# Performance work log

Measured on AMD Instinct MI355X. Metric: run time of the kernel, lower is better.

## Reference

```python
import jax, jax.numpy as jnp
import numpy as np

B, S, HID = 2, 2048, 2048
NH, NKV, HD = 32, 8, 64
ROPE_THETA = 10000.0
SCALE = HD ** -0.5
GROUP = NH // NKV


def setup_inputs() -> dict:
    key = jax.random.key(0)
    k1, k2, k3 = jax.random.split(key, 3)
    positions = jnp.tile(jnp.arange(S, dtype=jnp.int32), (B, 1))  # [B,S]
    hidden_states = jax.random.normal(k1, (B, S, HID), dtype=jnp.float32)
    Wqkv = jax.random.normal(k2, (HID, (NH + 2 * NKV) * HD), dtype=jnp.float32) * (HID ** -0.5)
    Wo = jax.random.normal(k3, (NH * HD, HID), dtype=jnp.float32) * ((NH * HD) ** -0.5)
    return {"positions": positions, "hidden_states": hidden_states, "Wqkv": Wqkv, "Wo": Wo}


def _apply_rope(x, cos, sin):
    # x: [B,S,H,HD]; cos/sin: [B,S,1,HD/2]  (neox style: rotate halves)
    x1, x2 = x[..., : HD // 2], x[..., HD // 2 :]
    return jnp.concatenate([x1 * cos - x2 * sin, x2 * cos + x1 * sin], axis=-1)


def reference(positions, hidden_states, Wqkv, Wo):
    # QKV projection (bias=False)
    qkv = hidden_states @ Wqkv  # [B,S,(NH+2*NKV)*HD]
    q, k, v = jnp.split(qkv, [NH * HD, (NH + NKV) * HD], axis=-1)
    q = q.reshape(B, S, NH, HD)
    k = k.reshape(B, S, NKV, HD)
    v = v.reshape(B, S, NKV, HD)

    # neox-style RoPE
    inv_freq = 1.0 / (ROPE_THETA ** (jnp.arange(0, HD, 2, dtype=jnp.float32) / HD))  # [HD/2]
    freqs = positions.astype(jnp.float32)[..., None] * inv_freq  # [B,S,HD/2]
    cos = jnp.cos(freqs)[:, :, None, :]
    sin = jnp.sin(freqs)[:, :, None, :]
    q = _apply_rope(q, cos, sin)
    k = _apply_rope(k, cos, sin)

    # GQA: expand KV heads to match query heads
    k = jnp.repeat(k, GROUP, axis=2)  # [B,S,NH,HD]
    v = jnp.repeat(v, GROUP, axis=2)

    # causal attention
    scores = jnp.einsum("bqhd,bkhd->bhqk", q, k) * SCALE  # [B,NH,S,S]
    causal = jnp.tril(jnp.ones((S, S), dtype=bool))
    scores = jnp.where(causal, scores, jnp.finfo(scores.dtype).min)
    probs = jax.nn.softmax(scores, axis=-1)
    attn = jnp.einsum("bhqk,bkhd->bqhd", probs, v).reshape(B, S, NH * HD)

    return attn @ Wo  # [B,S,HID]
```

## Files before the change

kernel.cpp:

```cpp
#include <hip/hip_runtime.h>
#include <hip/hip_bf16.h>
#include <math.h>

#define SEQ 2048
#define HIDDEN 2048
#define NHEAD 32
#define NKVH 8
#define HD 64
#define QKVW 3072

typedef __bf16 bf16_t;
typedef __bf16 bf16x8 __attribute__((ext_vector_type(8)));
typedef __bf16 bf16x4 __attribute__((ext_vector_type(4)));
typedef float f32x4 __attribute__((ext_vector_type(4)));

__device__ __forceinline__ void gld_lds16(const bf16_t* g, bf16_t* l) {
  __builtin_amdgcn_global_load_lds((const __attribute__((address_space(1))) void*)g,
                                   (__attribute__((address_space(3))) void*)l, 16, 0, 0);
}

__global__ __launch_bounds__(256) void k_fill(float* __restrict__ out, int n, float v) {
  int i = blockIdx.x * 256 + threadIdx.x;
  if (i < n) out[i] = v;
}

__global__ __launch_bounds__(256) void k_cvt(const float* __restrict__ in,
                                             bf16_t* __restrict__ out, int n4) {
  int i = blockIdx.x * 256 + threadIdx.x;
  if (i >= n4) return;
  float4 v = ((const float4*)in)[i];
  bf16x4 o;
  o[0] = (bf16_t)v.x; o[1] = (bf16_t)v.y; o[2] = (bf16_t)v.z; o[3] = (bf16_t)v.w;
  ((bf16x4*)out)[i] = o;
}

__global__ __launch_bounds__(256) void k_tconv(const float* __restrict__ in,
                                               bf16_t* __restrict__ out, int R, int C) {
  __shared__ float t[64][65];
  const int c0 = blockIdx.x * 64, r0 = blockIdx.y * 64;
#pragma unroll
  for (int i = 0; i < 16; ++i) {
    int idx = threadIdx.x + i * 256;
    int r = idx >> 6, c = idx & 63;
    t[r][c] = in[(size_t)(r0 + r) * C + c0 + c];
  }
  __syncthreads();
#pragma unroll
  for (int i = 0; i < 16; ++i) {
    int idx = threadIdx.x + i * 256;
    int nr = idx >> 6, kc = idx & 63;
    out[(size_t)(c0 + nr) * R + r0 + kc] = (bf16_t)t[kc][nr];
  }
}

template <typename OutT>
__global__ __launch_bounds__(256) void k_gemm(const bf16_t* __restrict__ A,
                                              const bf16_t* __restrict__ Bt,
                                              OutT* __restrict__ C,
                                              int M, int N, int K) {
  __shared__ __align__(16) bf16_t As[128 * 32];
  __shared__ __align__(16) bf16_t Bs[128 * 32];
  const int tid  = threadIdx.x;
  const int wave = tid >> 6, lane = tid & 63;
  const int lr = lane & 15, quad = lane >> 4;
  const int mtile = blockIdx.y * 128, ntile = blockIdx.x * 128;
  const int wm = (wave & 1) * 64, wn = (wave >> 1) * 64;

  const int srow = tid >> 2, scol = (tid & 3) * 8;
  const bf16_t* aG = A  + (size_t)(mtile + srow) * K + scol;
  const bf16_t* bG = Bt + (size_t)(ntile + srow) * K + scol;
  const size_t rstep = (size_t)64 * K;
  bf16_t* lA0 = As + tid * 8; bf16_t* lA1 = As + 2048 + tid * 8;
  bf16_t* lB0 = Bs + tid * 8; bf16_t* lB1 = Bs + 2048 + tid * 8;

  f32x4 acc[4][4];
  const f32x4 z4 = {0.f, 0.f, 0.f, 0.f};
#pragma unroll
  for (int mf = 0; mf < 4; ++mf)
#pragma unroll
    for (int nf = 0; nf < 4; ++nf) acc[mf][nf] = z4;

  for (int kt = 0; kt < K; kt += 32) {
    __syncthreads();
    gld_lds16(aG + kt,         lA0);
    gld_lds16(aG + rstep + kt, lA1);
    gld_lds16(bG + kt,         lB0);
    gld_lds16(bG + rstep + kt, lB1);
    __syncthreads();
    bf16x8 af[4], bfr[4];
#pragma unroll
    for (int mf = 0; mf < 4; ++mf)
      af[mf] = *(const bf16x8*)(As + (wm + mf * 16 + lr) * 32 + quad * 8);
#pragma unroll
    for (int nf = 0; nf < 4; ++nf)
      bfr[nf] = *(const bf16x8*)(Bs + (wn + nf * 16 + lr) * 32 + quad * 8);
#pragma unroll
    for (int mf = 0; mf < 4; ++mf)
#pragma unroll
      for (int nf = 0; nf < 4; ++nf)
        acc[mf][nf] = __builtin_amdgcn_mfma_f32_16x16x32_bf16(af[mf], bfr[nf], acc[mf][nf], 0, 0, 0);
  }
#pragma unroll
  for (int mf = 0; mf < 4; ++mf)
#pragma unroll
    for (int nf = 0; nf < 4; ++nf)
#pragma unroll
      for (int r = 0; r < 4; ++r)
        C[(size_t)(mtile + wm + mf * 16 + quad * 4 + r) * N + ntile + wn + nf * 16 + lr] =
            (OutT)acc[mf][nf][r];
}

__global__ __launch_bounds__(256) void k_gemm_qkv(const bf16_t* __restrict__ A,
                                                  const bf16_t* __restrict__ Bt,
                                                  const unsigned* __restrict__ pos,
                                                  bf16_t* __restrict__ ql,
                                                  bf16_t* __restrict__ kl,
                                                  bf16_t* __restrict__ vbuf,
                                                  int K) {
  __shared__ __align__(16) bf16_t As[128 * 32];
  __shared__ __align__(16) bf16_t Bs[128 * 32];
  const int tid  = threadIdx.x;
  const int wave = tid >> 6, lane = tid & 63;
  const int lr = lane & 15, quad = lane >> 4;
  const int mtile = blockIdx.y * 128, ntile = blockIdx.x * 128;
  const int wm = (wave & 1) * 64, wn = (wave >> 1) * 64;

  const int srow = tid >> 2, scol = (tid & 3) * 8;
  const bf16_t* aG = A  + (size_t)(mtile + srow) * K + scol;
  const bf16_t* bG = Bt + (size_t)(ntile + srow) * K + scol;
  const size_t rstep = (size_t)64 * K;
  bf16_t* lA0 = As + tid * 8; bf16_t* lA1 = As + 2048 + tid * 8;
  bf16_t* lB0 = Bs + tid * 8; bf16_t* lB1 = Bs + 2048 + tid * 8;

  f32x4 acc[4][4];
  const f32x4 z4 = {0.f, 0.f, 0.f, 0.f};
#pragma unroll
  for (int mf = 0; mf < 4; ++mf)
#pragma unroll
    for (int nf = 0; nf < 4; ++nf) acc[mf][nf] = z4;

  for (int kt = 0; kt < K; kt += 32) {
    __syncthreads();
    gld_lds16(aG + kt,         lA0);
    gld_lds16(aG + rstep + kt, lA1);
    gld_lds16(bG + kt,         lB0);
    gld_lds16(bG + rstep + kt, lB1);
    __syncthreads();
    bf16x8 af[4], bfr[4];
#pragma unroll
    for (int mf = 0; mf < 4; ++mf)
      af[mf] = *(const bf16x8*)(As + (wm + mf * 16 + lr) * 32 + quad * 8);
#pragma unroll
    for (int nf = 0; nf < 4; ++nf)
      bfr[nf] = *(const bf16x8*)(Bs + (wn + nf * 16 + lr) * 32 + quad * 8);
#pragma unroll
    for (int mf = 0; mf < 4; ++mf)
#pragma unroll
      for (int nf = 0; nf < 4; ++nf)
        acc[mf][nf] = __builtin_amdgcn_mfma_f32_16x16x32_bf16(af[mf], bfr[nf], acc[mf][nf], 0, 0, 0);
  }

  const int colbase = ntile + wn;
  if (colbase < 2560) {
    const bool isq = colbase < 2048;
    const int h = isq ? (colbase >> 6) : ((colbase - 2048) >> 6);
    bf16_t* obase = isq ? ql : kl;
    const int nhh = isq ? NHEAD : NKVH;
    const float scale = isq ? 0.125f : 1.0f;
    const float invf0 = exp2f((float)lr * -0.41524101186092029f);
    const float invf1 = exp2f((float)(lr + 16) * -0.41524101186092029f);
#pragma unroll
    for (int mf = 0; mf < 4; ++mf)
#pragma unroll
      for (int r = 0; r < 4; ++r) {
        int row = mtile + wm + mf * 16 + quad * 4 + r;
        int b = row >> 11, s = row & 2047;
        unsigned u = pos[row];
        float p = (u >= 0x3F800000u) ? __uint_as_float(u) : (float)(int)u;
#pragma unroll
        for (int nf = 0; nf < 2; ++nf) {
          float x1 = acc[mf][nf][r], x2 = acc[mf][nf + 2][r];
          float sn, cs;
          sincosf(p * (nf ? invf1 : invf0), &sn, &cs);
          size_t base = (((size_t)b * nhh + h) * SEQ + s) * HD + nf * 16 + lr;
          obase[base]      = (bf16_t)((x1 * cs - x2 * sn) * scale);
          obase[base + 32] = (bf16_t)((x2 * cs + x1 * sn) * scale);
        }
      }
  } else {
    const int kvh = (colbase - 2560) >> 6;
#pragma unroll
    for (int mf = 0; mf < 4; ++mf)
#pragma unroll
      for (int nf = 0; nf < 4; ++nf)
#pragma unroll
        for (int r = 0; r < 4; ++r) {
          int row = mtile + wm + mf * 16 + quad * 4 + r;
          vbuf[(size_t)row * 512 + kvh * 64 + nf * 16 + lr] = (bf16_t)acc[mf][nf][r];
        }
  }
}

__global__ __launch_bounds__(256) void k_vtrans(const bf16_t* __restrict__ vbuf,
                                                bf16_t* __restrict__ vt) {
  __shared__ bf16_t t[64][66];
  const int s0 = blockIdx.x * 64;
  const int bk = blockIdx.y;
  const int b = bk >> 3, kvh = bk & 7;
#pragma unroll
  for (int i = 0; i < 16; ++i) {
    int idx = threadIdx.x + i * 256;
    int r = idx >> 6, c = idx & 63;
    t[r][c] = vbuf[((size_t)b * SEQ + s0 + r) * 512 + kvh * 64 + c];
  }
  __syncthreads();
#pragma unroll
  for (int i = 0; i < 16; ++i) {
    int idx = threadIdx.x + i * 256;
    int dr = idx >> 6, sc = idx & 63;
    vt[(((size_t)b * NKVH + kvh) * HD + dr) * SEQ + s0 + sc] = t[sc][dr];
  }
}

__global__ __launch_bounds__(256, 4) void k_attn(const bf16_t* __restrict__ ql,
                                                 const bf16_t* __restrict__ kl,
                                                 const bf16_t* __restrict__ vt,
                                                 bf16_t* __restrict__ attn) {
  __shared__ __align__(16) bf16_t Ks[2][64 * 64];
  __shared__ __align__(16) bf16_t Vs[2][64 * 64];
  __shared__ __align__(16) bf16_t P[4][16 * 64];
  const int pairp = blockIdx.x;
  const int bh = blockIdx.y;
  const int b = bh >> 5, h = bh & 31;
  const int kvh = h >> 2;
  const int wave = threadIdx.x >> 6, lane = threadIdx.x & 63;
  const int lr = lane & 15, quad = lane >> 4;
  const int lhi = lane >> 3, llo = lane & 7;
  const int gsw = llo ^ lhi;
  const bf16_t* qp = ql + ((size_t)b * NHEAD + h) * SEQ * HD;
  const bf16_t* kp = kl + ((size_t)b * NKVH + kvh) * SEQ * HD;
  const bf16_t* vp = vt + ((size_t)b * NKVH + kvh) * HD * SEQ;
  const f32x4 z4 = {0.f, 0.f, 0.f, 0.f};

  auto stage = [&](int buf, int kt) {
    const int k0s = kt * 64;
    const bf16_t* kbase = kp + (size_t)k0s * HD;
#pragma unroll
    for (int j = 0; j < 2; ++j) {
      int key = (wave * 2 + j) * 8 + lhi;
      gld_lds16(kbase + (size_t)key * HD + gsw * 8, &Ks[buf][(wave * 2 + j) * 512 + lane * 8]);
    }
#pragma unroll
    for (int j = 0; j < 2; ++j) {
      int hd = wave * 16 + j * 8 + lhi;
      gld_lds16(vp + (size_t)hd * SEQ + k0s + gsw * 8, &Vs[buf][(wave * 16 + j * 8) * 64 + lane * 8]);
    }
  };

#pragma unroll
  for (int seg = 0; seg < 2; ++seg) {
    const int tile = seg ? pairp : 31 - pairp;
    const int q0 = tile * 64 + wave * 16;

    bf16x8 aq[2];
#pragma unroll
    for (int ks = 0; ks < 2; ++ks)
      aq[ks] = *(const bf16x8*)(qp + (size_t)(q0 + lr) * HD + ks * 32 + quad * 8);

    f32x4 acc[4];
    float mrow[4], lrow[4];
#pragma unroll
    for (int nf = 0; nf < 4; ++nf) acc[nf] = z4;
#pragma unroll
    for (int r = 0; r < 4; ++r) { mrow[r] = -1e30f; lrow[r] = 0.f; }

    const int ntiles = tile + 1;
    int cur = 0;
    stage(0, 0);
    __syncthreads();

    for (int kt = 0; kt < ntiles; ++kt) {
      const int k0 = kt * 64;
      if (kt + 1 < ntiles) stage(cur ^ 1, kt + 1);

      bf16x8 bk[2][4];
#pragma unroll
      for (int ks = 0; ks < 2; ++ks)
#pragma unroll
        for (int nh = 0; nh < 4; ++nh)
          bk[ks][nh] = *(const bf16x8*)(&Ks[cur][(nh * 16 + lr) * 64 + (((ks * 4 + quad) ^ (lr & 7)) << 3)]);
      f32x4 sc[4];
#pragma unroll
      for (int nh = 0; nh < 4; ++nh) {
        sc[nh] = __builtin_amdgcn_mfma_f32_16x16x32_bf16(aq[0], bk[0][nh], z4, 0, 0, 0);
        sc[nh] = __builtin_amdgcn_mfma_f32_16x16x32_bf16(aq[1], bk[1][nh], sc[nh], 0, 0, 0);
      }

      if (kt == ntiles - 1) {
#pragma unroll
        for (int nh = 0; nh < 4; ++nh)
#pragma unroll
          for (int r = 0; r < 4; ++r) {
            int qg = q0 + quad * 4 + r;
            int kg = k0 + nh * 16 + lr;
            if (kg > qg) sc[nh][r] = -1e30f;
          }
      }

      float rm[4];
#pragma unroll
      for (int r = 0; r < 4; ++r)
        rm[r] = fmaxf(fmaxf(sc[0][r], sc[1][r]), fmaxf(sc[2][r], sc[3][r]));
#pragma unroll
      for (int off = 1; off < 16; off <<= 1)
#pragma unroll
        for (int r = 0; r < 4; ++r) rm[r] = fmaxf(rm[r], __shfl_xor(rm[r], off, 64));
      int ng = (rm[0] <= mrow[0] + 8.f) & (rm[1] <= mrow[1] + 8.f) &
               (rm[2] <= mrow[2] + 8.f) & (rm[3] <= mrow[3] + 8.f);
      if (!__all(ng)) {
#pragma unroll
        for (int r = 0; r < 4; ++r) {
          float mn = fmaxf(mrow[r], rm[r]);
          float al = __expf(mrow[r] - mn);
          mrow[r] = mn;
          lrow[r] *= al;
#pragma unroll
          for (int nf = 0; nf < 4; ++nf) acc[nf][r] *= al;
        }
      }
#pragma unroll
      for (int nh = 0; nh < 4; ++nh)
#pragma unroll
        for (int r = 0; r < 4; ++r) sc[nh][r] = __expf(sc[nh][r] - mrow[r]);
#pragma unroll
      for (int r = 0; r < 4; ++r)
        lrow[r] += (sc[0][r] + sc[1][r]) + (sc[2][r] + sc[3][r]);
#pragma unroll
      for (int nh = 0; nh < 4; ++nh)
#pragma unroll
        for (int r = 0; r < 4; ++r) {
          int row = quad * 4 + r;
          int cg = (nh * 2 + (lr >> 3)) ^ (row & 7);
          P[wave][row * 64 + (cg << 3) + (lr & 7)] = (bf16_t)sc[nh][r];
        }
      __asm__ volatile("s_waitcnt lgkmcnt(0)" ::: "memory");
      bf16x8 pa[2], bv[2][4];
#pragma unroll
      for (int kg = 0; kg < 2; ++kg)
        pa[kg] = *(const bf16x8*)(&P[wave][lr * 64 + (((kg * 4 + quad) ^ (lr & 7)) << 3)]);
#pragma unroll
      for (int kg = 0; kg < 2; ++kg)
#pragma unroll
        for (int nf = 0; nf < 4; ++nf)
          bv[kg][nf] = *(const bf16x8*)(&Vs[cur][(nf * 16 + lr) * 64 + (((kg * 4 + quad) ^ (lr & 7)) << 3)]);
      __asm__ volatile("" ::: "memory");
#pragma unroll
      for (int nf = 0; nf < 4; ++nf) {
        acc[nf] = __builtin_amdgcn_mfma_f32_16x16x32_bf16(pa[0], bv[0][nf], acc[nf], 0, 0, 0);
        acc[nf] = __builtin_amdgcn_mfma_f32_16x16x32_bf16(pa[1], bv[1][nf], acc[nf], 0, 0, 0);
      }
      __syncthreads();
      cur ^= 1;
    }

#pragma unroll
    for (int off = 1; off < 16; off <<= 1)
#pragma unroll
      for (int r = 0; r < 4; ++r) lrow[r] += __shfl_xor(lrow[r], off, 64);

#pragma unroll
    for (int r = 0; r < 4; ++r) {
      float inv = 1.f / lrow[r];
      int row = q0 + quad * 4 + r;
#pragma unroll
      for (int nf = 0; nf < 4; ++nf)
        attn[((size_t)b * SEQ + row) * HIDDEN + h * HD + nf * 16 + lr] =
            (bf16_t)(acc[nf][r] * inv);
    }
  }
}

extern "C" void kernel_launch(void* const* d_in, const int* in_sizes, int n_in,
                              void* d_out, int out_size, void* d_ws, size_t ws_size,
                              hipStream_t stream) {
  float* out = (float*)d_out;

  if (n_in != 4) { k_fill<<<dim3(32768), dim3(256), 0, stream>>>(out, 8388608, 222.0f); return; }
  if (out_size != 8388608) { k_fill<<<dim3(32768), dim3(256), 0, stream>>>(out, 8388608, 111.0f); return; }
  if (ws_size < (size_t)109051904) { k_fill<<<dim3(32768), dim3(256), 0, stream>>>(out, 8388608, 777.0f); return; }

  int ord[4] = {0, 1, 2, 3};
  for (int i = 1; i < 4; ++i)
    for (int j = i; j > 0 && in_sizes[ord[j]] > in_sizes[ord[j - 1]]; --j) {
      int t = ord[j]; ord[j] = ord[j - 1]; ord[j - 1] = t;
    }
  const float*    hidden    = (const float*)d_in[ord[0]];
  const float*    wqkv      = (const float*)d_in[ord[1]];
  const float*    wo        = (const float*)d_in[ord[2]];
  const unsigned* positions = (const unsigned*)d_in[ord[3]];

  char* ws = (char*)d_ws;
  bf16_t* hidB  = (bf16_t*)(ws + 0);
  bf16_t* wqkvT = (bf16_t*)(ws + 16777216);
  bf16_t* woT   = (bf16_t*)(ws + 29360128);
  bf16_t* vbuf  = (bf16_t*)(ws + 37748736);
  bf16_t* ql    = (bf16_t*)(ws + 62914560);
  bf16_t* kl    = (bf16_t*)(ws + 79691776);
  bf16_t* vt    = (bf16_t*)(ws + 83886080);
  bf16_t* attnb = (bf16_t*)(ws + 88080384);

  k_cvt<<<dim3(8192), dim3(256), 0, stream>>>(hidden, hidB, 2097152);
  k_tconv<<<dim3(48, 32), dim3(256), 0, stream>>>(wqkv, wqkvT, 2048, 3072);
  k_tconv<<<dim3(32, 32), dim3(256), 0, stream>>>(wo, woT, 2048, 2048);
  k_gemm_qkv<<<dim3(24, 32), dim3(256), 0, stream>>>(hidB, wqkvT, positions, ql, kl, vbuf, 2048);
  k_vtrans<<<dim3(32, 16), dim3(256), 0, stream>>>(vbuf, vt);
  k_attn<<<dim3(16, 64), dim3(256), 0, stream>>>(ql, kl, vt, attnb);
  k_gemm<float><<<dim3(16, 32), dim3(256), 0, stream>>>(attnb, woT, out, 4096, 2048, 2048);
}
```

Baseline: 337.5 us.

## Replace both GEMMs with 256x256-tile 8-wave double-buffered swizzled kernel

```diff
diff --git a/kernel.cpp b/kernel.cpp
--- a/kernel.cpp
+++ b/kernel.cpp
@@ -7,7 +7,6 @@
 #define NHEAD 32
 #define NKVH 8
 #define HD 64
-#define QKVW 3072
 
 typedef __bf16 bf16_t;
 typedef __bf16 bf16x8 __attribute__((ext_vector_type(8)));
@@ -18,6 +17,13 @@
   __builtin_amdgcn_global_load_lds((const __attribute__((address_space(1))) void*)g,
                                    (__attribute__((address_space(3))) void*)l, 16, 0, 0);
 }
+
+#define BARX()                              \
+  do {                                      \
+    __builtin_amdgcn_sched_barrier(0);      \
+    __builtin_amdgcn_s_barrier();           \
+    __builtin_amdgcn_sched_barrier(0);      \
+  } while (0)
 
 __global__ __launch_bounds__(256) void k_fill(float* __restrict__ out, int n, float v) {
   int i = blockIdx.x * 256 + threadIdx.x;
@@ -53,151 +59,173 @@
   }
 }
 
-template <typename OutT>
-__global__ __launch_bounds__(256) void k_gemm(const bf16_t* __restrict__ A,
-                                              const bf16_t* __restrict__ Bt,
-                                              OutT* __restrict__ C,
-                                              int M, int N, int K) {
-  __shared__ __align__(16) bf16_t As[128 * 32];
-  __shared__ __align__(16) bf16_t Bs[128 * 32];
-  const int tid  = threadIdx.x;
-  const int wave = tid >> 6, lane = tid & 63;
-  const int lr = lane & 15, quad = lane >> 4;
-  const int mtile = blockIdx.y * 128, ntile = blockIdx.x * 128;
-  const int wm = (wave & 1) * 64, wn = (wave >> 1) * 64;
-
-  const int srow = tid >> 2, scol = (tid & 3) * 8;
-  const bf16_t* aG = A  + (size_t)(mtile + srow) * K + scol;
-  const bf16_t* bG = Bt + (size_t)(ntile + srow) * K + scol;
-  const size_t rstep = (size_t)64 * K;
-  bf16_t* lA0 = As + tid * 8; bf16_t* lA1 = As + 2048 + tid * 8;
-  bf16_t* lB0 = Bs + tid * 8; bf16_t* lB1 = Bs + 2048 + tid * 8;
-
-  f32x4 acc[4][4];
-  const f32x4 z4 = {0.f, 0.f, 0.f, 0.f};
-#pragma unroll
-  for (int mf = 0; mf < 4; ++mf)
-#pragma unroll
-    for (int nf = 0; nf < 4; ++nf) acc[mf][nf] = z4;
-
-  for (int kt = 0; kt < K; kt += 32) {
-    __syncthreads();
-    gld_lds16(aG + kt,         lA0);
-    gld_lds16(aG + rstep + kt, lA1);
-    gld_lds16(bG + kt,         lB0);
-    gld_lds16(bG + rstep + kt, lB1);
-    __syncthreads();
-    bf16x8 af[4], bfr[4];
-#pragma unroll
-    for (int mf = 0; mf < 4; ++mf)
-      af[mf] = *(const bf16x8*)(As + (wm + mf * 16 + lr) * 32 + quad * 8);
-#pragma unroll
-    for (int nf = 0; nf < 4; ++nf)
-      bfr[nf] = *(const bf16x8*)(Bs + (wn + nf * 16 + lr) * 32 + quad * 8);
-#pragma unroll
-    for (int mf = 0; mf < 4; ++mf)
-#pragma unroll
-      for (int nf = 0; nf < 4; ++nf)
-        acc[mf][nf] = __builtin_amdgcn_mfma_f32_16x16x32_bf16(af[mf], bfr[nf], acc[mf][nf], 0, 0, 0);
-  }
-#pragma unroll
-  for (int mf = 0; mf < 4; ++mf)
-#pragma unroll
-    for (int nf = 0; nf < 4; ++nf)
-#pragma unroll
-      for (int r = 0; r < 4; ++r)
-        C[(size_t)(mtile + wm + mf * 16 + quad * 4 + r) * N + ntile + wn + nf * 16 + lr] =
-            (OutT)acc[mf][nf][r];
-}
-
-__global__ __launch_bounds__(256) void k_gemm_qkv(const bf16_t* __restrict__ A,
+template <int EPI, int NC>
+__global__ __launch_bounds__(512, 2) void k_gemm8(const bf16_t* __restrict__ A,
                                                   const bf16_t* __restrict__ Bt,
                                                   const unsigned* __restrict__ pos,
+                                                  float* __restrict__ Cf,
                                                   bf16_t* __restrict__ ql,
                                                   bf16_t* __restrict__ kl,
-                                                  bf16_t* __restrict__ vbuf,
-                                                  int K) {
-  __shared__ __align__(16) bf16_t As[128 * 32];
-  __shared__ __align__(16) bf16_t Bs[128 * 32];
-  const int tid  = threadIdx.x;
+                                                  bf16_t* __restrict__ vbuf) {
+  __shared__ __align__(16) bf16_t As[2][256 * 64];
+  __shared__ __align__(16) bf16_t Bs[2][256 * 64];
+  const int nwg = gridDim.x;
+  const int L = blockIdx.x;
+  const int wg = (L & 7) * (nwg >> 3) + (L >> 3);
+  const int NBX = NC / 256;
+  const int bx = wg % NBX, by = wg / NBX;
+  const int mtile = by * 256, ntile = bx * 256;
+  const int tid = threadIdx.x;
   const int wave = tid >> 6, lane = tid & 63;
+  const int wm = wave >> 2, wn = wave & 3;
   const int lr = lane & 15, quad = lane >> 4;
-  const int mtile = blockIdx.y * 128, ntile = blockIdx.x * 128;
-  const int wm = (wave & 1) * 64, wn = (wave >> 1) * 64;
-
-  const int srow = tid >> 2, scol = (tid & 3) * 8;
-  const bf16_t* aG = A  + (size_t)(mtile + srow) * K + scol;
-  const bf16_t* bG = Bt + (size_t)(ntile + srow) * K + scol;
-  const size_t rstep = (size_t)64 * K;
-  bf16_t* lA0 = As + tid * 8; bf16_t* lA1 = As + 2048 + tid * 8;
-  bf16_t* lB0 = Bs + tid * 8; bf16_t* lB1 = Bs + 2048 + tid * 8;
-
-  f32x4 acc[4][4];
+  const int scol = ((lane & 7) * 8) ^ (((lane >> 5) & 1) << 4);
+  const int srow8 = (lane >> 3) & 7;
+
+  auto stageA = [&](int buf, int h, int kt) {
+#pragma unroll
+    for (int j = 0; j < 2; ++j) {
+      int rt = h * 128 + (wave * 2 + j) * 8 + srow8;
+      gld_lds16(A + (size_t)(mtile + rt) * 2048 + kt * 64 + scol,
+                &As[buf][h * 8192 + (wave * 2 + j) * 512 + lane * 8]);
+    }
+  };
+  auto stageB = [&](int buf, int h, int kt) {
+#pragma unroll
+    for (int j = 0; j < 2; ++j) {
+      int rt = h * 128 + (wave * 2 + j) * 8 + srow8;
+      gld_lds16(Bt + (size_t)(ntile + rt) * 2048 + kt * 64 + scol,
+                &Bs[buf][h * 8192 + (wave * 2 + j) * 512 + lane * 8]);
+    }
+  };
+  auto rdA = [&](int buf, int mhalf, int mf, int kk) -> bf16x8 {
+    int row = wm * 128 + mhalf * 64 + mf * 16 + lr;
+    int col = (kk * 32 + quad * 8) ^ (((row >> 2) & 1) << 4);
+    return *(const bf16x8*)(&As[buf][row * 64 + col]);
+  };
+  auto rdB = [&](int buf, int nhalf, int nf, int kk) -> bf16x8 {
+    int row = wn * 64 + nhalf * 32 + nf * 16 + lr;
+    int col = (kk * 32 + quad * 8) ^ (((row >> 2) & 1) << 4);
+    return *(const bf16x8*)(&Bs[buf][row * 64 + col]);
+  };
+
+  f32x4 acc[8][4];
   const f32x4 z4 = {0.f, 0.f, 0.f, 0.f};
 #pragma unroll
-  for (int mf = 0; mf < 4; ++mf)
-#pragma unroll
-    for (int nf = 0; nf < 4; ++nf) acc[mf][nf] = z4;
-
-  for (int kt = 0; kt < K; kt += 32) {
-    __syncthreads();
-    gld_lds16(aG + kt,         lA0);
-    gld_lds16(aG + rstep + kt, lA1);
-    gld_lds16(bG + kt,         lB0);
-    gld_lds16(bG + rstep + kt, lB1);
-    __syncthreads();
-    bf16x8 af[4], bfr[4];
+  for (int mi = 0; mi < 8; ++mi)
+#pragma unroll
+    for (int ni = 0; ni < 4; ++ni) acc[mi][ni] = z4;
+
+  auto mmaq = [&](bf16x8 (&a)[4][2], bf16x8 (&bb)[2][2], int mo, int no) {
+    __builtin_amdgcn_s_setprio(1);
 #pragma unroll
     for (int mf = 0; mf < 4; ++mf)
-      af[mf] = *(const bf16x8*)(As + (wm + mf * 16 + lr) * 32 + quad * 8);
-#pragma unroll
-    for (int nf = 0; nf < 4; ++nf)
-      bfr[nf] = *(const bf16x8*)(Bs + (wn + nf * 16 + lr) * 32 + quad * 8);
-#pragma unroll
-    for (int mf = 0; mf < 4; ++mf)
-#pragma unroll
-      for (int nf = 0; nf < 4; ++nf)
-        acc[mf][nf] = __builtin_amdgcn_mfma_f32_16x16x32_bf16(af[mf], bfr[nf], acc[mf][nf], 0, 0, 0);
-  }
-
-  const int colbase = ntile + wn;
-  if (colbase < 2560) {
-    const bool isq = colbase < 2048;
-    const int h = isq ? (colbase >> 6) : ((colbase - 2048) >> 6);
-    bf16_t* obase = isq ? ql : kl;
-    const int nhh = isq ? NHEAD : NKVH;
-    const float scale = isq ? 0.125f : 1.0f;
-    const float invf0 = exp2f((float)lr * -0.41524101186092029f);
-    const float invf1 = exp2f((float)(lr + 16) * -0.41524101186092029f);
-#pragma unroll
-    for (int mf = 0; mf < 4; ++mf)
-#pragma unroll
-      for (int r = 0; r < 4; ++r) {
-        int row = mtile + wm + mf * 16 + quad * 4 + r;
-        int b = row >> 11, s = row & 2047;
-        unsigned u = pos[row];
-        float p = (u >= 0x3F800000u) ? __uint_as_float(u) : (float)(int)u;
-#pragma unroll
-        for (int nf = 0; nf < 2; ++nf) {
-          float x1 = acc[mf][nf][r], x2 = acc[mf][nf + 2][r];
-          float sn, cs;
-          sincosf(p * (nf ? invf1 : invf0), &sn, &cs);
-          size_t base = (((size_t)b * nhh + h) * SEQ + s) * HD + nf * 16 + lr;
-          obase[base]      = (bf16_t)((x1 * cs - x2 * sn) * scale);
-          obase[base + 32] = (bf16_t)((x2 * cs + x1 * sn) * scale);
+#pragma unroll
+      for (int nf = 0; nf < 2; ++nf)
+#pragma unroll
+        for (int kk = 0; kk < 2; ++kk)
+          acc[mo + mf][no + nf] = __builtin_amdgcn_mfma_f32_16x16x32_bf16(
+              a[mf][kk], bb[nf][kk], acc[mo + mf][no + nf], 0, 0, 0);
+    __builtin_amdgcn_s_setprio(0);
+  };
+
+  stageA(0, 0, 0); stageA(0, 1, 0); stageB(0, 0, 0); stageB(0, 1, 0);
+  stageA(1, 0, 1); stageA(1, 1, 1);
+  asm volatile("s_waitcnt vmcnt(4)" ::: "memory");
+  BARX();
+
+  for (int i = 0; i < 16; ++i) {
+#pragma unroll
+    for (int half = 0; half < 2; ++half) {
+      const int buf = half;
+      int tb = 2 * i + 1 + half; if (tb > 31) tb = 31;
+      int ta = 2 * i + 2 + half; if (ta > 31) ta = 31;
+      bf16x8 a0[4][2], a1[4][2], b[2][2];
+#pragma unroll
+      for (int mf = 0; mf < 4; ++mf)
+#pragma unroll
+        for (int kk = 0; kk < 2; ++kk) a0[mf][kk] = rdA(buf, 0, mf, kk);
+#pragma unroll
+      for (int nf = 0; nf < 2; ++nf)
+#pragma unroll
+        for (int kk = 0; kk < 2; ++kk) b[nf][kk] = rdB(buf, 0, nf, kk);
+      stageB(buf ^ 1, 0, tb); stageB(buf ^ 1, 1, tb);
+      BARX();
+      mmaq(a0, b, 0, 0);
+      BARX();
+#pragma unroll
+      for (int mf = 0; mf < 4; ++mf)
+#pragma unroll
+        for (int kk = 0; kk < 2; ++kk) a1[mf][kk] = rdA(buf, 1, mf, kk);
+      BARX();
+      mmaq(a1, b, 4, 0);
+      BARX();
+#pragma unroll
+      for (int nf = 0; nf < 2; ++nf)
+#pragma unroll
+        for (int kk = 0; kk < 2; ++kk) b[nf][kk] = rdB(buf, 1, nf, kk);
+      BARX();
+      mmaq(a1, b, 4, 2);
+      BARX();
+      stageA(buf, 0, ta); stageA(buf, 1, ta);
+      asm volatile("s_waitcnt vmcnt(4)" ::: "memory");
+      BARX();
+      mmaq(a0, b, 0, 2);
+      BARX();
+    }
+  }
+  asm volatile("s_waitcnt vmcnt(0)" ::: "memory");
+  BARX();
+
+  if constexpr (EPI == 0) {
+#pragma unroll
+    for (int mi = 0; mi < 8; ++mi)
+#pragma unroll
+      for (int ni = 0; ni < 4; ++ni)
+#pragma unroll
+        for (int r = 0; r < 4; ++r)
+          Cf[(size_t)(mtile + wm * 128 + mi * 16 + quad * 4 + r) * NC +
+             ntile + wn * 64 + ni * 16 + lr] = acc[mi][ni][r];
+  } else {
+    const int colbase = ntile + wn * 64;
+    if (colbase < 2560) {
+      const bool isq = colbase < 2048;
+      const int h = isq ? (colbase >> 6) : ((colbase - 2048) >> 6);
+      bf16_t* obase = isq ? ql : kl;
+      const int nhh = isq ? NHEAD : NKVH;
+      const float scale = isq ? 0.125f : 1.0f;
+      const float invf0 = exp2f((float)lr * -0.41524101186092029f);
+      const float invf1 = exp2f((float)(lr + 16) * -0.41524101186092029f);
+#pragma unroll
+      for (int mi = 0; mi < 8; ++mi)
+#pragma unroll
+        for (int r = 0; r < 4; ++r) {
+          int row = mtile + wm * 128 + mi * 16 + quad * 4 + r;
+          int b = row >> 11, s = row & 2047;
+          unsigned u = pos[row];
+          float p = (u >= 0x3F800000u) ? __uint_as_float(u) : (float)(int)u;
+#pragma unroll
+          for (int nf = 0; nf < 2; ++nf) {
+            float x1 = acc[mi][nf][r], x2 = acc[mi][nf + 2][r];
+            float sn, cs;
+            sincosf(p * (nf ? invf1 : invf0), &sn, &cs);
+            size_t base = (((size_t)b * nhh + h) * SEQ + s) * HD + nf * 16 + lr;
+            obase[base]      = (bf16_t)((x1 * cs - x2 * sn) * scale);
+            obase[base + 32] = (bf16_t)((x2 * cs + x1 * sn) * scale);
+          }
         }
-      }
-  } else {
-    const int kvh = (colbase - 2560) >> 6;
-#pragma unroll
-    for (int mf = 0; mf < 4; ++mf)
-#pragma unroll
-      for (int nf = 0; nf < 4; ++nf)
-#pragma unroll
-        for (int r = 0; r < 4; ++r) {
-          int row = mtile + wm + mf * 16 + quad * 4 + r;
-          vbuf[(size_t)row * 512 + kvh * 64 + nf * 16 + lr] = (bf16_t)acc[mf][nf][r];
-        }
+    } else {
+      const int kvh = (colbase - 2560) >> 6;
+#pragma unroll
+      for (int mi = 0; mi < 8; ++mi)
+#pragma unroll
+        for (int ni = 0; ni < 4; ++ni)
+#pragma unroll
+          for (int r = 0; r < 4; ++r) {
+            int row = mtile + wm * 128 + mi * 16 + quad * 4 + r;
+            vbuf[(size_t)row * 512 + kvh * 64 + ni * 16 + lr] = (bf16_t)acc[mi][ni][r];
+          }
+    }
   }
 }
 
@@ -412,8 +440,8 @@
   k_cvt<<<dim3(8192), dim3(256), 0, stream>>>(hidden, hidB, 2097152);
   k_tconv<<<dim3(48, 32), dim3(256), 0, stream>>>(wqkv, wqkvT, 2048, 3072);
   k_tconv<<<dim3(32, 32), dim3(256), 0, stream>>>(wo, woT, 2048, 2048);
-  k_gemm_qkv<<<dim3(24, 32), dim3(256), 0, stream>>>(hidB, wqkvT, positions, ql, kl, vbuf, 2048);
+  k_gemm8<1, 3072><<<dim3(192), dim3(512), 0, stream>>>(hidB, wqkvT, positions, nullptr, ql, kl, vbuf);
   k_vtrans<<<dim3(32, 16), dim3(256), 0, stream>>>(vbuf, vt);
   k_attn<<<dim3(16, 64), dim3(256), 0, stream>>>(ql, kl, vt, attnb);
-  k_gemm<float><<<dim3(16, 32), dim3(256), 0, stream>>>(attnb, woT, out, 4096, 2048, 2048);
-}
+  k_gemm8<0, 2048><<<dim3(128), dim3(512), 0, stream>>>(attnb, woT, nullptr, out, nullptr, nullptr, nullptr);
+}
```

Result: slower. 394.2 us (+16.8%).
